# Optimization experiments

Measured on AMD Instinct MI355X. Metric: run time of the kernel, lower is better.

## Reference

```python
import jax, jax.numpy as jnp
import numpy as np

B, S, D, H = 2, 2048, 1024, 16
HD = D // H
NEG_INF = jnp.finfo(jnp.float32).min


def setup_inputs() -> dict:
    key = jax.random.key(0)
    ks = jax.random.split(key, 6)
    s = 1.0 / np.sqrt(D)
    return {
        'x': jax.random.normal(ks[0], (B, S, D), dtype=jnp.float32),
        'Wq': jax.random.normal(ks[1], (D, D), dtype=jnp.float32) * s,
        'Wk': jax.random.normal(ks[2], (D, D), dtype=jnp.float32) * s,
        'Wv': jax.random.normal(ks[3], (D, D), dtype=jnp.float32) * s,
        'Wo': jax.random.normal(ks[4], (D, D), dtype=jnp.float32) * s,
        'bo': jnp.zeros((D,), dtype=jnp.float32),
    }


def reference(x, Wq, Wk, Wv, Wo, bo):
    b, s, _ = x.shape
    scale = HD ** -0.5
    # Q/K/V projections: einsum('bnd,di->bni') == x @ W
    def proj(W):
        return jnp.einsum('bnd,di->bni', x, W).reshape(b, s, H, HD).transpose(0, 2, 1, 3)
    Q, K, V = proj(Wq), proj(Wk), proj(Wv)  # [b,h,s,hd]
    scores = jnp.einsum('bhnd,bhmd->bhnm', Q, K) * scale  # [b,h,s,s]
    causal = jnp.tril(jnp.ones((s, s), dtype=bool))
    scores = jnp.where(causal[None, None], scores, NEG_INF)
    attn = jax.nn.softmax(scores, axis=-1)
    ctx = jnp.einsum('bhnm,bhmd->bhnd', attn, V)
    ctx = ctx.transpose(0, 2, 1, 3).reshape(b, s, D)
    # nn.Linear: ctx @ Wo.T + bo
    return jnp.einsum('bnd,od->bno', ctx, Wo) + bo
```

## Files before the change

kernel.cpp:

```cpp
#include <hip/hip_runtime.h>

#define B_  2
#define S_  2048
#define D_  1024
#define H_  16
#define HD_ 64
#define M_  (B_*S_)

typedef __attribute__((ext_vector_type(8))) short s16x8;
typedef __attribute__((ext_vector_type(4))) float f32x4;
typedef __attribute__((ext_vector_type(16))) float f32x16;

__device__ __forceinline__ unsigned short f2bf(float f) {
  unsigned int u = __builtin_bit_cast(unsigned int, f);
  u += 0x7fffu + ((u >> 16) & 1u);
  return (unsigned short)(u >> 16);
}

__device__ __forceinline__ void gload_lds16(const unsigned short* g, unsigned short* l) {
  __builtin_amdgcn_global_load_lds((const __attribute__((address_space(1))) void*)g,
                                   (__attribute__((address_space(3))) void*)l, 16, 0, 0);
}

__global__ void cvt_kernel(const float* __restrict__ in, unsigned short* __restrict__ out, int n4) {
  int i = blockIdx.x * blockDim.x + threadIdx.x;
  if (i >= n4) return;
  float4 v = reinterpret_cast<const float4*>(in)[i];
  ushort4 o;
  o.x = f2bf(v.x); o.y = f2bf(v.y); o.z = f2bf(v.z); o.w = f2bf(v.w);
  reinterpret_cast<ushort4*>(out)[i] = o;
}

__global__ void transpose_cvt3(const float* __restrict__ W0, const float* __restrict__ W1,
                               const float* __restrict__ W2, unsigned short* __restrict__ dstBase) {
  __shared__ float tile[32][33];
  const float* in = blockIdx.z == 0 ? W0 : (blockIdx.z == 1 ? W1 : W2);
  unsigned short* out = dstBase + (size_t)blockIdx.z * 1024 * 1024;
  const int bx = blockIdx.x, by = blockIdx.y, tx = threadIdx.x;
  const int x = bx * 32 + tx;
  for (int j = threadIdx.y; j < 32; j += 8)
    tile[j][tx] = in[(by * 32 + j) * 1024 + x];
  __syncthreads();
  const int xo = by * 32 + tx;
  for (int j = threadIdx.y; j < 32; j += 8)
    out[(bx * 32 + j) * 1024 + xo] = f2bf(tile[tx][j]);
}

#define BM 128
#define BN 128
#define BK 64

__global__ __launch_bounds__(256, 4) void gemm_bt(
    const unsigned short* __restrict__ A,
    const unsigned short* __restrict__ Bt,
    void* __restrict__ out0, void* __restrict__ out1, void* __restrict__ out2,
    const float* __restrict__ bias,
    const int mode, const float qscale)
{
  __shared__ unsigned short As[BM * BK];
  __shared__ unsigned short Bs[BN * BK];

  const int t    = threadIdx.x;
  const int lane = t & 63;
  const int wid  = t >> 6;
  const int l15  = lane & 15;
  const int g    = lane >> 4;
  const int wm   = wid >> 1;
  const int wn   = wid & 1;

  const int n0 = blockIdx.x * BN;
  const int m0 = blockIdx.y * BM;

  const int lrow = lane >> 3;
  const int lcol = ((lane & 7) ^ lrow) * 8;
  const int rsw  = l15 & 7;

  f32x4 acc[4][4];
#pragma unroll
  for (int i = 0; i < 4; ++i)
#pragma unroll
    for (int j = 0; j < 4; ++j)
      acc[i][j] = (f32x4){0.f, 0.f, 0.f, 0.f};

  for (int kt = 0; kt < 1024 / BK; ++kt) {
    const int k0 = kt * BK;
#pragma unroll
    for (int p = 0; p < 4; ++p) {
      const int c = p * 4 + wid;
      const int row = c * 8 + lrow;
      gload_lds16(&A[(size_t)(m0 + row) * 1024 + k0 + lcol], &As[c * 512]);
      gload_lds16(&Bt[(size_t)(n0 + row) * 1024 + k0 + lcol], &Bs[c * 512]);
    }
    __syncthreads();

#pragma unroll
    for (int kk = 0; kk < 2; ++kk) {
      s16x8 af[4], bf[4];
#pragma unroll
      for (int mi = 0; mi < 4; ++mi)
        af[mi] = *reinterpret_cast<const s16x8*>(
            &As[(wm * 64 + mi * 16 + l15) * BK + (((4 * kk + g) ^ rsw) * 8)]);
#pragma unroll
      for (int ni = 0; ni < 4; ++ni)
        bf[ni] = *reinterpret_cast<const s16x8*>(
            &Bs[(wn * 64 + ni * 16 + l15) * BK + (((4 * kk + g) ^ rsw) * 8)]);
#pragma unroll
      for (int mi = 0; mi < 4; ++mi)
#pragma unroll
        for (int ni = 0; ni < 4; ++ni)
          acc[mi][ni] = __builtin_amdgcn_mfma_f32_16x16x32_bf16(af[mi], bf[ni], acc[mi][ni], 0, 0, 0);
    }
    __syncthreads();
  }

  if (mode == 0) {
    const int sel = n0 >> 10;
    const int nl0 = n0 & 1023;
    if (sel < 2) {
      unsigned short* outb = (unsigned short*)(sel == 0 ? out0 : out1);
      const float sc = (sel == 0) ? qscale : 1.0f;
#pragma unroll
      for (int mi = 0; mi < 4; ++mi) {
#pragma unroll
        for (int ni = 0; ni < 4; ++ni) {
          const int n = nl0 + wn * 64 + ni * 16 + l15;
          const int h = n >> 6, hd = n & 63;
#pragma unroll
          for (int r = 0; r < 4; ++r) {
            const int m = m0 + wm * 64 + mi * 16 + 4 * g + r;
            const int b = m >> 11, s = m & 2047;
            outb[(((b * H_ + h) * S_) + s) * HD_ + hd] = f2bf(acc[mi][ni][r] * sc);
          }
        }
      }
    } else {
      unsigned short* outb = (unsigned short*)out2;
#pragma unroll
      for (int mi = 0; mi < 4; ++mi) {
#pragma unroll
        for (int ni = 0; ni < 4; ++ni) {
          const int n = nl0 + wn * 64 + ni * 16 + l15;
          const int h = n >> 6, hd = n & 63;
          const int m = m0 + wm * 64 + mi * 16 + 4 * g;
          const int b = m >> 11, s = m & 2047;
          ushort4 o;
          o.x = f2bf(acc[mi][ni][0]);
          o.y = f2bf(acc[mi][ni][1]);
          o.z = f2bf(acc[mi][ni][2]);
          o.w = f2bf(acc[mi][ni][3]);
          *reinterpret_cast<ushort4*>(&outb[(((b * H_ + h) * HD_) + hd) * S_ + s]) = o;
        }
      }
    }
  } else {
    float* outf = (float*)out0;
#pragma unroll
    for (int mi = 0; mi < 4; ++mi) {
#pragma unroll
      for (int ni = 0; ni < 4; ++ni) {
        const int n = n0 + wn * 64 + ni * 16 + l15;
        const float bv = bias[n];
#pragma unroll
        for (int r = 0; r < 4; ++r) {
          const int m = m0 + wm * 64 + mi * 16 + 4 * g + r;
          outf[m * 1024 + n] = acc[mi][ni][r] + bv;
        }
      }
    }
  }
}

__global__ __launch_bounds__(256) void attn_kernel(
    const unsigned short* __restrict__ Q,
    const unsigned short* __restrict__ K,
    const unsigned short* __restrict__ VT,
    unsigned short* __restrict__ Ctx)
{
  __shared__ unsigned short Kl[2][64 * 64];
  __shared__ unsigned short Vl[2][64 * 64];
  __shared__ unsigned short Pl[4][2][32][40];

  const int t    = threadIdx.x;
  const int lane = t & 63;
  const int w    = t >> 6;
  const int q    = lane & 31;
  const int hi   = lane >> 5;

  const int bh = blockIdx.x;
  const long base  = (long)bh * S_ * HD_;
  const long vbase = (long)bh * HD_ * S_;

  const int srow = lane >> 3;
  const int scol = ((lane & 7) ^ srow) * 8;
  const int swz  = (q & 7) * 8;

  for (int hp = 0; hp < 2; ++hp) {
    const int qb  = hp == 0 ? 15 - (int)blockIdx.y : (int)blockIdx.y;
    const int q0w = qb * 128 + w * 32;

    s16x8 qf[4];
#pragma unroll
    for (int s = 0; s < 4; ++s)
      qf[s] = *reinterpret_cast<const s16x8*>(&Q[base + (long)(q0w + q) * HD_ + 16 * s + 8 * hi]);

    f32x16 ctx0, ctx1;
#pragma unroll
    for (int r = 0; r < 16; ++r) { ctx0[r] = 0.f; ctx1[r] = 0.f; }
    float m_run = -1e30f, l_run = 0.f;

    const int nt = 2 * qb + 2;

#pragma unroll
    for (int p = 0; p < 2; ++p) {
      const int c = 2 * w + p;
      gload_lds16(&K[base + (long)(c * 8 + srow) * HD_ + scol], &Kl[0][c * 512]);
      gload_lds16(&VT[vbase + (long)(c * 8 + srow) * S_ + scol], &Vl[0][c * 512]);
    }
    __syncthreads();

    for (int kt = 0; kt < nt; ++kt) {
      const int cur  = kt & 1;
      const int kv64 = kt * 64;

      if (kt + 1 < nt) {
        const int nk = kv64 + 64;
#pragma unroll
        for (int p = 0; p < 2; ++p) {
          const int c = 2 * w + p;
          gload_lds16(&K[base + (long)(nk + c * 8 + srow) * HD_ + scol], &Kl[cur ^ 1][c * 512]);
          gload_lds16(&VT[vbase + (long)(c * 8 + srow) * S_ + nk + scol], &Vl[cur ^ 1][c * 512]);
        }
      }

      if (kv64 <= q0w + 31) {
        f32x16 sa0, sa1;
#pragma unroll
        for (int r = 0; r < 16; ++r) { sa0[r] = 0.f; sa1[r] = 0.f; }
        __builtin_amdgcn_s_setprio(1);
#pragma unroll
        for (int s = 0; s < 4; ++s) {
          const s16x8 kb0 = *reinterpret_cast<const s16x8*>(&Kl[cur][(q) * 64 + ((16 * s + 8 * hi) ^ swz)]);
          sa0 = __builtin_amdgcn_mfma_f32_32x32x16_bf16(kb0, qf[s], sa0, 0, 0, 0);
        }
#pragma unroll
        for (int s = 0; s < 4; ++s) {
          const s16x8 kb1 = *reinterpret_cast<const s16x8*>(&Kl[cur][(32 + q) * 64 + ((16 * s + 8 * hi) ^ swz)]);
          sa1 = __builtin_amdgcn_mfma_f32_32x32x16_bf16(kb1, qf[s], sa1, 0, 0, 0);
        }
        __builtin_amdgcn_s_setprio(0);

        if (kv64 + 64 > q0w) {
#pragma unroll
          for (int r = 0; r < 16; ++r) {
            const int kl = (r & 3) + 8 * (r >> 2) + 4 * hi;
            if (kv64 + kl > q0w + q)      sa0[r] = -1e30f;
            if (kv64 + 32 + kl > q0w + q) sa1[r] = -1e30f;
          }
        }

        float mx;
        {
          float a0 = fmaxf(fmaxf(sa0[0], sa0[1]), fmaxf(sa0[2], sa0[3]));
          float a1 = fmaxf(fmaxf(sa0[4], sa0[5]), fmaxf(sa0[6], sa0[7]));
          float a2 = fmaxf(fmaxf(sa0[8], sa0[9]), fmaxf(sa0[10], sa0[11]));
          float a3 = fmaxf(fmaxf(sa0[12], sa0[13]), fmaxf(sa0[14], sa0[15]));
          float b0 = fmaxf(fmaxf(sa1[0], sa1[1]), fmaxf(sa1[2], sa1[3]));
          float b1 = fmaxf(fmaxf(sa1[4], sa1[5]), fmaxf(sa1[6], sa1[7]));
          float b2 = fmaxf(fmaxf(sa1[8], sa1[9]), fmaxf(sa1[10], sa1[11]));
          float b3 = fmaxf(fmaxf(sa1[12], sa1[13]), fmaxf(sa1[14], sa1[15]));
          mx = fmaxf(fmaxf(fmaxf(a0, a1), fmaxf(a2, a3)), fmaxf(fmaxf(b0, b1), fmaxf(b2, b3)));
          mx = fmaxf(mx, __shfl_xor(mx, 32));
        }
        if (mx > m_run + 8.f) {
          const float alpha = __builtin_amdgcn_exp2f(m_run - mx);
          m_run = mx;
          l_run *= alpha;
#pragma unroll
          for (int r = 0; r < 16; ++r) { ctx0[r] *= alpha; ctx1[r] *= alpha; }
        }

        float p0[16], p1[16];
#pragma unroll
        for (int r = 0; r < 16; ++r) {
          p0[r] = __builtin_amdgcn_exp2f(sa0[r] - m_run);
          p1[r] = __builtin_amdgcn_exp2f(sa1[r] - m_run);
        }
        float ps;
        {
          float s0 = ((p0[0] + p0[1]) + (p0[2] + p0[3])) + ((p0[4] + p0[5]) + (p0[6] + p0[7]));
          float s1 = ((p0[8] + p0[9]) + (p0[10] + p0[11])) + ((p0[12] + p0[13]) + (p0[14] + p0[15]));
          float s2 = ((p1[0] + p1[1]) + (p1[2] + p1[3])) + ((p1[4] + p1[5]) + (p1[6] + p1[7]));
          float s3 = ((p1[8] + p1[9]) + (p1[10] + p1[11])) + ((p1[12] + p1[13]) + (p1[14] + p1[15]));
          ps = (s0 + s1) + (s2 + s3);
          ps += __shfl_xor(ps, 32);
        }
        l_run += ps;

#pragma unroll
        for (int c = 0; c < 4; ++c) {
          unsigned int pk01, pk23;
          asm("v_cvt_pk_bf16_f32 %0, %1, %2" : "=v"(pk01) : "v"(p0[4 * c + 0]), "v"(p0[4 * c + 1]));
          asm("v_cvt_pk_bf16_f32 %0, %1, %2" : "=v"(pk23) : "v"(p0[4 * c + 2]), "v"(p0[4 * c + 3]));
          uint2 pr; pr.x = pk01; pr.y = pk23;
          *reinterpret_cast<uint2*>(&Pl[w][0][q][8 * c + 4 * hi]) = pr;
        }
#pragma unroll
        for (int c = 0; c < 4; ++c) {
          unsigned int pk01, pk23;
          asm("v_cvt_pk_bf16_f32 %0, %1, %2" : "=v"(pk01) : "v"(p1[4 * c + 0]), "v"(p1[4 * c + 1]));
          asm("v_cvt_pk_bf16_f32 %0, %1, %2" : "=v"(pk23) : "v"(p1[4 * c + 2]), "v"(p1[4 * c + 3]));
          uint2 pr; pr.x = pk01; pr.y = pk23;
          *reinterpret_cast<uint2*>(&Pl[w][1][q][8 * c + 4 * hi]) = pr;
        }

        __builtin_amdgcn_s_setprio(1);
#pragma unroll
        for (int kc = 0; kc < 4; ++kc) {
          const s16x8 pf = *reinterpret_cast<const s16x8*>(&Pl[w][kc >> 1][q][16 * (kc & 1) + 8 * hi]);
          const s16x8 v0 = *reinterpret_cast<const s16x8*>(&Vl[cur][(q) * 64 + ((16 * kc + 8 * hi) ^ swz)]);
          ctx0 = __builtin_amdgcn_mfma_f32_32x32x16_bf16(v0, pf, ctx0, 0, 0, 0);
          const s16x8 v1 = *reinterpret_cast<const s16x8*>(&Vl[cur][(32 + q) * 64 + ((16 * kc + 8 * hi) ^ swz)]);
          ctx1 = __builtin_amdgcn_mfma_f32_32x32x16_bf16(v1, pf, ctx1, 0, 0, 0);
        }
        __builtin_amdgcn_s_setprio(0);
      }

      __syncthreads();
    }

    const int b = bh >> 4, h = bh & 15;
    const float inv = 1.f / l_run;
    unsigned short* orow = &Ctx[((long)b * S_ + q0w + q) * D_ + h * 64];
#pragma unroll
    for (int c = 0; c < 4; ++c) {
      ushort4 o0, o1;
      o0.x = f2bf(ctx0[4 * c] * inv);     o0.y = f2bf(ctx0[4 * c + 1] * inv);
      o0.z = f2bf(ctx0[4 * c + 2] * inv); o0.w = f2bf(ctx0[4 * c + 3] * inv);
      o1.x = f2bf(ctx1[4 * c] * inv);     o1.y = f2bf(ctx1[4 * c + 1] * inv);
      o1.z = f2bf(ctx1[4 * c + 2] * inv); o1.w = f2bf(ctx1[4 * c + 3] * inv);
      *reinterpret_cast<ushort4*>(&orow[8 * c + 4 * hi])      = o0;
      *reinterpret_cast<ushort4*>(&orow[32 + 8 * c + 4 * hi]) = o1;
    }
  }
}

extern "C" void kernel_launch(void* const* d_in, const int* in_sizes, int n_in,
                              void* d_out, int out_size, void* d_ws, size_t ws_size,
                              hipStream_t stream) {
  const float* x  = (const float*)d_in[0];
  const float* Wq = (const float*)d_in[1];
  const float* Wk = (const float*)d_in[2];
  const float* Wv = (const float*)d_in[3];
  const float* Wo = (const float*)d_in[4];
  const float* bo = (const float*)d_in[5];
  float* out = (float*)d_out;

  char* ws = (char*)d_ws;
  const size_t MB = 1024 * 1024;
  unsigned short* xb  = (unsigned short*)(ws + 0 * MB);
  unsigned short* WT  = (unsigned short*)(ws + 8 * MB);
  unsigned short* Wob = (unsigned short*)(ws + 14 * MB);
  unsigned short* Qb  = (unsigned short*)(ws + 16 * MB);
  unsigned short* Kb  = (unsigned short*)(ws + 24 * MB);
  unsigned short* VTb = (unsigned short*)(ws + 32 * MB);
  unsigned short* Cx  = (unsigned short*)(ws + 40 * MB);

  cvt_kernel<<<(M_ * D_ / 4 + 255) / 256, 256, 0, stream>>>(x, xb, M_ * D_ / 4);
  cvt_kernel<<<(D_ * D_ / 4 + 255) / 256, 256, 0, stream>>>(Wo, Wob, D_ * D_ / 4);
  transpose_cvt3<<<dim3(32, 32, 3), dim3(32, 8), 0, stream>>>(Wq, Wk, Wv, WT);

  gemm_bt<<<dim3(3 * D_ / BN, M_ / BM), 256, 0, stream>>>(
      xb, WT, (void*)Qb, (void*)Kb, (void*)VTb, nullptr, 0, 0.18033688011112042f);

  attn_kernel<<<dim3(B_ * H_, 8), 256, 0, stream>>>(Qb, Kb, VTb, Cx);

  gemm_bt<<<dim3(D_ / BN, M_ / BM), 256, 0, stream>>>(
      Cx, Wob, (void*)out, nullptr, nullptr, bo, 1, 1.0f);
}
```

Measured before the change: 127.9 us.

## Split long causal query blocks across two workgroups with a softmax merge kernel

```diff
diff --git a/kernel.cpp b/kernel.cpp
--- a/kernel.cpp
+++ b/kernel.cpp
@@ -15,6 +15,10 @@
   unsigned int u = __builtin_bit_cast(unsigned int, f);
   u += 0x7fffu + ((u >> 16) & 1u);
   return (unsigned short)(u >> 16);
+}
+__device__ __forceinline__ float bf2f(unsigned short h) {
+  unsigned int u = ((unsigned int)h) << 16;
+  return __builtin_bit_cast(float, u);
 }
 
 __device__ __forceinline__ void gload_lds16(const unsigned short* g, unsigned short* l) {
@@ -174,11 +178,16 @@
     const unsigned short* __restrict__ Q,
     const unsigned short* __restrict__ K,
     const unsigned short* __restrict__ VT,
-    unsigned short* __restrict__ Ctx)
+    unsigned short* __restrict__ Ctx,
+    unsigned short* __restrict__ pctx,
+    float* __restrict__ pml)
 {
   __shared__ unsigned short Kl[2][64 * 64];
   __shared__ unsigned short Vl[2][64 * 64];
   __shared__ unsigned short Pl[4][2][32][40];
+
+  static const unsigned char QBv[24] = {15,15,7,14,14,13,13,6,12,12,11,11,5,10,10,9,9,4,8,8,3,2,1,0};
+  static const signed char   HFv[24] = {0,1,-1,0,1,0,1,-1,0,1,0,1,-1,0,1,0,1,-1,0,1,-1,-1,-1,-1};
 
   const int t    = threadIdx.x;
   const int lane = t & 63;
@@ -187,147 +196,149 @@
   const int hi   = lane >> 5;
 
   const int bh = blockIdx.x;
+  const int qb = QBv[blockIdx.y];
+  const int hf = HFv[blockIdx.y];
   const long base  = (long)bh * S_ * HD_;
   const long vbase = (long)bh * HD_ * S_;
+  const int q0w = qb * 128 + w * 32;
+
+  int ktBeg, ktEnd;
+  if (hf < 0) { ktBeg = 0; ktEnd = 2 * qb + 2; }
+  else        { ktBeg = hf * (qb + 1); ktEnd = ktBeg + qb + 1; }
 
   const int srow = lane >> 3;
   const int scol = ((lane & 7) ^ srow) * 8;
   const int swz  = (q & 7) * 8;
 
-  for (int hp = 0; hp < 2; ++hp) {
-    const int qb  = hp == 0 ? 15 - (int)blockIdx.y : (int)blockIdx.y;
-    const int q0w = qb * 128 + w * 32;
-
-    s16x8 qf[4];
-#pragma unroll
-    for (int s = 0; s < 4; ++s)
-      qf[s] = *reinterpret_cast<const s16x8*>(&Q[base + (long)(q0w + q) * HD_ + 16 * s + 8 * hi]);
-
-    f32x16 ctx0, ctx1;
-#pragma unroll
-    for (int r = 0; r < 16; ++r) { ctx0[r] = 0.f; ctx1[r] = 0.f; }
-    float m_run = -1e30f, l_run = 0.f;
-
-    const int nt = 2 * qb + 2;
-
-#pragma unroll
-    for (int p = 0; p < 2; ++p) {
-      const int c = 2 * w + p;
-      gload_lds16(&K[base + (long)(c * 8 + srow) * HD_ + scol], &Kl[0][c * 512]);
-      gload_lds16(&VT[vbase + (long)(c * 8 + srow) * S_ + scol], &Vl[0][c * 512]);
-    }
+  s16x8 qf[4];
+#pragma unroll
+  for (int s = 0; s < 4; ++s)
+    qf[s] = *reinterpret_cast<const s16x8*>(&Q[base + (long)(q0w + q) * HD_ + 16 * s + 8 * hi]);
+
+  f32x16 ctx0, ctx1;
+#pragma unroll
+  for (int r = 0; r < 16; ++r) { ctx0[r] = 0.f; ctx1[r] = 0.f; }
+  float m_run = -1e30f, l_run = 0.f;
+
+#pragma unroll
+  for (int p = 0; p < 2; ++p) {
+    const int c = 2 * w + p;
+    gload_lds16(&K[base + (long)(ktBeg * 64 + c * 8 + srow) * HD_ + scol], &Kl[0][c * 512]);
+    gload_lds16(&VT[vbase + (long)(c * 8 + srow) * S_ + ktBeg * 64 + scol], &Vl[0][c * 512]);
+  }
+  __syncthreads();
+
+  for (int kt = ktBeg; kt < ktEnd; ++kt) {
+    const int cur  = (kt - ktBeg) & 1;
+    const int kv64 = kt * 64;
+
+    if (kt + 1 < ktEnd) {
+      const int nk = (kt + 1) * 64;
+#pragma unroll
+      for (int p = 0; p < 2; ++p) {
+        const int c = 2 * w + p;
+        gload_lds16(&K[base + (long)(nk + c * 8 + srow) * HD_ + scol], &Kl[cur ^ 1][c * 512]);
+        gload_lds16(&VT[vbase + (long)(c * 8 + srow) * S_ + nk + scol], &Vl[cur ^ 1][c * 512]);
+      }
+    }
+
+    if (kv64 <= q0w + 31) {
+      f32x16 sa0, sa1;
+#pragma unroll
+      for (int r = 0; r < 16; ++r) { sa0[r] = 0.f; sa1[r] = 0.f; }
+      __builtin_amdgcn_s_setprio(1);
+#pragma unroll
+      for (int s = 0; s < 4; ++s) {
+        const s16x8 kb0 = *reinterpret_cast<const s16x8*>(&Kl[cur][(q) * 64 + ((16 * s + 8 * hi) ^ swz)]);
+        sa0 = __builtin_amdgcn_mfma_f32_32x32x16_bf16(kb0, qf[s], sa0, 0, 0, 0);
+      }
+#pragma unroll
+      for (int s = 0; s < 4; ++s) {
+        const s16x8 kb1 = *reinterpret_cast<const s16x8*>(&Kl[cur][(32 + q) * 64 + ((16 * s + 8 * hi) ^ swz)]);
+        sa1 = __builtin_amdgcn_mfma_f32_32x32x16_bf16(kb1, qf[s], sa1, 0, 0, 0);
+      }
+      __builtin_amdgcn_s_setprio(0);
+
+      if (kv64 + 64 > q0w) {
+#pragma unroll
+        for (int r = 0; r < 16; ++r) {
+          const int kl = (r & 3) + 8 * (r >> 2) + 4 * hi;
+          if (kv64 + kl > q0w + q)      sa0[r] = -1e30f;
+          if (kv64 + 32 + kl > q0w + q) sa1[r] = -1e30f;
+        }
+      }
+
+      float mx;
+      {
+        float a0 = fmaxf(fmaxf(sa0[0], sa0[1]), fmaxf(sa0[2], sa0[3]));
+        float a1 = fmaxf(fmaxf(sa0[4], sa0[5]), fmaxf(sa0[6], sa0[7]));
+        float a2 = fmaxf(fmaxf(sa0[8], sa0[9]), fmaxf(sa0[10], sa0[11]));
+        float a3 = fmaxf(fmaxf(sa0[12], sa0[13]), fmaxf(sa0[14], sa0[15]));
+        float b0 = fmaxf(fmaxf(sa1[0], sa1[1]), fmaxf(sa1[2], sa1[3]));
+        float b1 = fmaxf(fmaxf(sa1[4], sa1[5]), fmaxf(sa1[6], sa1[7]));
+        float b2 = fmaxf(fmaxf(sa1[8], sa1[9]), fmaxf(sa1[10], sa1[11]));
+        float b3 = fmaxf(fmaxf(sa1[12], sa1[13]), fmaxf(sa1[14], sa1[15]));
+        mx = fmaxf(fmaxf(fmaxf(a0, a1), fmaxf(a2, a3)), fmaxf(fmaxf(b0, b1), fmaxf(b2, b3)));
+        mx = fmaxf(mx, __shfl_xor(mx, 32));
+      }
+      if (mx > m_run + 8.f) {
+        const float alpha = __builtin_amdgcn_exp2f(m_run - mx);
+        m_run = mx;
+        l_run *= alpha;
+#pragma unroll
+        for (int r = 0; r < 16; ++r) { ctx0[r] *= alpha; ctx1[r] *= alpha; }
+      }
+
+      float p0[16], p1[16];
+#pragma unroll
+      for (int r = 0; r < 16; ++r) {
+        p0[r] = __builtin_amdgcn_exp2f(sa0[r] - m_run);
+        p1[r] = __builtin_amdgcn_exp2f(sa1[r] - m_run);
+      }
+      float ps;
+      {
+        float s0 = ((p0[0] + p0[1]) + (p0[2] + p0[3])) + ((p0[4] + p0[5]) + (p0[6] + p0[7]));
+        float s1 = ((p0[8] + p0[9]) + (p0[10] + p0[11])) + ((p0[12] + p0[13]) + (p0[14] + p0[15]));
+        float s2 = ((p1[0] + p1[1]) + (p1[2] + p1[3])) + ((p1[4] + p1[5]) + (p1[6] + p1[7]));
+        float s3 = ((p1[8] + p1[9]) + (p1[10] + p1[11])) + ((p1[12] + p1[13]) + (p1[14] + p1[15]));
+        ps = (s0 + s1) + (s2 + s3);
+        ps += __shfl_xor(ps, 32);
+      }
+      l_run += ps;
+
+#pragma unroll
+      for (int c = 0; c < 4; ++c) {
+        unsigned int pk01, pk23;
+        asm("v_cvt_pk_bf16_f32 %0, %1, %2" : "=v"(pk01) : "v"(p0[4 * c + 0]), "v"(p0[4 * c + 1]));
+        asm("v_cvt_pk_bf16_f32 %0, %1, %2" : "=v"(pk23) : "v"(p0[4 * c + 2]), "v"(p0[4 * c + 3]));
+        uint2 pr; pr.x = pk01; pr.y = pk23;
+        *reinterpret_cast<uint2*>(&Pl[w][0][q][8 * c + 4 * hi]) = pr;
+      }
+#pragma unroll
+      for (int c = 0; c < 4; ++c) {
+        unsigned int pk01, pk23;
+        asm("v_cvt_pk_bf16_f32 %0, %1, %2" : "=v"(pk01) : "v"(p1[4 * c + 0]), "v"(p1[4 * c + 1]));
+        asm("v_cvt_pk_bf16_f32 %0, %1, %2" : "=v"(pk23) : "v"(p1[4 * c + 2]), "v"(p1[4 * c + 3]));
+        uint2 pr; pr.x = pk01; pr.y = pk23;
+        *reinterpret_cast<uint2*>(&Pl[w][1][q][8 * c + 4 * hi]) = pr;
+      }
+
+      __builtin_amdgcn_s_setprio(1);
+#pragma unroll
+      for (int kc = 0; kc < 4; ++kc) {
+        const s16x8 pf = *reinterpret_cast<const s16x8*>(&Pl[w][kc >> 1][q][16 * (kc & 1) + 8 * hi]);
+        const s16x8 v0 = *reinterpret_cast<const s16x8*>(&Vl[cur][(q) * 64 + ((16 * kc + 8 * hi) ^ swz)]);
+        ctx0 = __builtin_amdgcn_mfma_f32_32x32x16_bf16(v0, pf, ctx0, 0, 0, 0);
+        const s16x8 v1 = *reinterpret_cast<const s16x8*>(&Vl[cur][(32 + q) * 64 + ((16 * kc + 8 * hi) ^ swz)]);
+        ctx1 = __builtin_amdgcn_mfma_f32_32x32x16_bf16(v1, pf, ctx1, 0, 0, 0);
+      }
+      __builtin_amdgcn_s_setprio(0);
+    }
+
     __syncthreads();
-
-    for (int kt = 0; kt < nt; ++kt) {
-      const int cur  = kt & 1;
-      const int kv64 = kt * 64;
-
-      if (kt + 1 < nt) {
-        const int nk = kv64 + 64;
-#pragma unroll
-        for (int p = 0; p < 2; ++p) {
-          const int c = 2 * w + p;
-          gload_lds16(&K[base + (long)(nk + c * 8 + srow) * HD_ + scol], &Kl[cur ^ 1][c * 512]);
-          gload_lds16(&VT[vbase + (long)(c * 8 + srow) * S_ + nk + scol], &Vl[cur ^ 1][c * 512]);
-        }
-      }
-
-      if (kv64 <= q0w + 31) {
-        f32x16 sa0, sa1;
-#pragma unroll
-        for (int r = 0; r < 16; ++r) { sa0[r] = 0.f; sa1[r] = 0.f; }
-        __builtin_amdgcn_s_setprio(1);
-#pragma unroll
-        for (int s = 0; s < 4; ++s) {
-          const s16x8 kb0 = *reinterpret_cast<const s16x8*>(&Kl[cur][(q) * 64 + ((16 * s + 8 * hi) ^ swz)]);
-          sa0 = __builtin_amdgcn_mfma_f32_32x32x16_bf16(kb0, qf[s], sa0, 0, 0, 0);
-        }
-#pragma unroll
-        for (int s = 0; s < 4; ++s) {
-          const s16x8 kb1 = *reinterpret_cast<const s16x8*>(&Kl[cur][(32 + q) * 64 + ((16 * s + 8 * hi) ^ swz)]);
-          sa1 = __builtin_amdgcn_mfma_f32_32x32x16_bf16(kb1, qf[s], sa1, 0, 0, 0);
-        }
-        __builtin_amdgcn_s_setprio(0);
-
-        if (kv64 + 64 > q0w) {
-#pragma unroll
-          for (int r = 0; r < 16; ++r) {
-            const int kl = (r & 3) + 8 * (r >> 2) + 4 * hi;
-            if (kv64 + kl > q0w + q)      sa0[r] = -1e30f;
-            if (kv64 + 32 + kl > q0w + q) sa1[r] = -1e30f;
-          }
-        }
-
-        float mx;
-        {
-          float a0 = fmaxf(fmaxf(sa0[0], sa0[1]), fmaxf(sa0[2], sa0[3]));
-          float a1 = fmaxf(fmaxf(sa0[4], sa0[5]), fmaxf(sa0[6], sa0[7]));
-          float a2 = fmaxf(fmaxf(sa0[8], sa0[9]), fmaxf(sa0[10], sa0[11]));
-          float a3 = fmaxf(fmaxf(sa0[12], sa0[13]), fmaxf(sa0[14], sa0[15]));
-          float b0 = fmaxf(fmaxf(sa1[0], sa1[1]), fmaxf(sa1[2], sa1[3]));
-          float b1 = fmaxf(fmaxf(sa1[4], sa1[5]), fmaxf(sa1[6], sa1[7]));
-          float b2 = fmaxf(fmaxf(sa1[8], sa1[9]), fmaxf(sa1[10], sa1[11]));
-          float b3 = fmaxf(fmaxf(sa1[12], sa1[13]), fmaxf(sa1[14], sa1[15]));
-          mx = fmaxf(fmaxf(fmaxf(a0, a1), fmaxf(a2, a3)), fmaxf(fmaxf(b0, b1), fmaxf(b2, b3)));
-          mx = fmaxf(mx, __shfl_xor(mx, 32));
-        }
-        if (mx > m_run + 8.f) {
-          const float alpha = __builtin_amdgcn_exp2f(m_run - mx);
-          m_run = mx;
-          l_run *= alpha;
-#pragma unroll
-          for (int r = 0; r < 16; ++r) { ctx0[r] *= alpha; ctx1[r] *= alpha; }
-        }
-
-        float p0[16], p1[16];
-#pragma unroll
-        for (int r = 0; r < 16; ++r) {
-          p0[r] = __builtin_amdgcn_exp2f(sa0[r] - m_run);
-          p1[r] = __builtin_amdgcn_exp2f(sa1[r] - m_run);
-        }
-        float ps;
-        {
-          float s0 = ((p0[0] + p0[1]) + (p0[2] + p0[3])) + ((p0[4] + p0[5]) + (p0[6] + p0[7]));
-          float s1 = ((p0[8] + p0[9]) + (p0[10] + p0[11])) + ((p0[12] + p0[13]) + (p0[14] + p0[15]));
-          float s2 = ((p1[0] + p1[1]) + (p1[2] + p1[3])) + ((p1[4] + p1[5]) + (p1[6] + p1[7]));
-          float s3 = ((p1[8] + p1[9]) + (p1[10] + p1[11])) + ((p1[12] + p1[13]) + (p1[14] + p1[15]));
-          ps = (s0 + s1) + (s2 + s3);
-          ps += __shfl_xor(ps, 32);
-        }
-        l_run += ps;
-
-#pragma unroll
-        for (int c = 0; c < 4; ++c) {
-          unsigned int pk01, pk23;
-          asm("v_cvt_pk_bf16_f32 %0, %1, %2" : "=v"(pk01) : "v"(p0[4 * c + 0]), "v"(p0[4 * c + 1]));
-          asm("v_cvt_pk_bf16_f32 %0, %1, %2" : "=v"(pk23) : "v"(p0[4 * c + 2]), "v"(p0[4 * c + 3]));
-          uint2 pr; pr.x = pk01; pr.y = pk23;
-          *reinterpret_cast<uint2*>(&Pl[w][0][q][8 * c + 4 * hi]) = pr;
-        }
-#pragma unroll
-        for (int c = 0; c < 4; ++c) {
-          unsigned int pk01, pk23;
-          asm("v_cvt_pk_bf16_f32 %0, %1, %2" : "=v"(pk01) : "v"(p1[4 * c + 0]), "v"(p1[4 * c + 1]));
-          asm("v_cvt_pk_bf16_f32 %0, %1, %2" : "=v"(pk23) : "v"(p1[4 * c + 2]), "v"(p1[4 * c + 3]));
-          uint2 pr; pr.x = pk01; pr.y = pk23;
-          *reinterpret_cast<uint2*>(&Pl[w][1][q][8 * c + 4 * hi]) = pr;
-        }
-
-        __builtin_amdgcn_s_setprio(1);
-#pragma unroll
-        for (int kc = 0; kc < 4; ++kc) {
-          const s16x8 pf = *reinterpret_cast<const s16x8*>(&Pl[w][kc >> 1][q][16 * (kc & 1) + 8 * hi]);
-          const s16x8 v0 = *reinterpret_cast<const s16x8*>(&Vl[cur][(q) * 64 + ((16 * kc + 8 * hi) ^ swz)]);
-          ctx0 = __builtin_amdgcn_mfma_f32_32x32x16_bf16(v0, pf, ctx0, 0, 0, 0);
-          const s16x8 v1 = *reinterpret_cast<const s16x8*>(&Vl[cur][(32 + q) * 64 + ((16 * kc + 8 * hi) ^ swz)]);
-          ctx1 = __builtin_amdgcn_mfma_f32_32x32x16_bf16(v1, pf, ctx1, 0, 0, 0);
-        }
-        __builtin_amdgcn_s_setprio(0);
-      }
-
-      __syncthreads();
-    }
-
+  }
+
+  if (hf < 0) {
     const int b = bh >> 4, h = bh & 15;
     const float inv = 1.f / l_run;
     unsigned short* orow = &Ctx[((long)b * S_ + q0w + q) * D_ + h * 64];
@@ -341,6 +352,66 @@
       *reinterpret_cast<ushort4*>(&orow[8 * c + 4 * hi])      = o0;
       *reinterpret_cast<ushort4*>(&orow[32 + 8 * c + 4 * hi]) = o1;
     }
+  } else {
+    const int sidx = ((bh << 3) + (qb - 8)) * 2 + hf;
+    const int rloc = w * 32 + q;
+    unsigned short* prow = &pctx[((long)sidx * 128 + rloc) * 64];
+#pragma unroll
+    for (int c = 0; c < 4; ++c) {
+      ushort4 o0, o1;
+      o0.x = f2bf(ctx0[4 * c]);     o0.y = f2bf(ctx0[4 * c + 1]);
+      o0.z = f2bf(ctx0[4 * c + 2]); o0.w = f2bf(ctx0[4 * c + 3]);
+      o1.x = f2bf(ctx1[4 * c]);     o1.y = f2bf(ctx1[4 * c + 1]);
+      o1.z = f2bf(ctx1[4 * c + 2]); o1.w = f2bf(ctx1[4 * c + 3]);
+      *reinterpret_cast<ushort4*>(&prow[8 * c + 4 * hi])      = o0;
+      *reinterpret_cast<ushort4*>(&prow[32 + 8 * c + 4 * hi]) = o1;
+    }
+    if (hi == 0) {
+      pml[((long)sidx * 128 + rloc) * 2]     = m_run;
+      pml[((long)sidx * 128 + rloc) * 2 + 1] = l_run;
+    }
+  }
+}
+
+__global__ __launch_bounds__(256) void merge_kernel(
+    const unsigned short* __restrict__ pctx,
+    const float* __restrict__ pml,
+    unsigned short* __restrict__ Ctx)
+{
+  const int unit = blockIdx.x;
+  const int bh = unit >> 3;
+  const int qb = (unit & 7) + 8;
+  const long s0 = (long)unit * 2, s1 = s0 + 1;
+
+  const int t   = threadIdx.x;
+  const int row = t >> 1;
+  const int hh  = t & 1;
+
+  const long r0 = s0 * 128 + row;
+  const long r1 = s1 * 128 + row;
+  const float m0 = pml[r0 * 2], l0 = pml[r0 * 2 + 1];
+  const float m1 = pml[r1 * 2], l1 = pml[r1 * 2 + 1];
+  const float M  = fmaxf(m0, m1);
+  const float a0 = __builtin_amdgcn_exp2f(m0 - M);
+  const float a1 = __builtin_amdgcn_exp2f(m1 - M);
+  const float inv = 1.f / (l0 * a0 + l1 * a1);
+
+  const unsigned short* c0p = &pctx[r0 * 64 + hh * 32];
+  const unsigned short* c1p = &pctx[r1 * 64 + hh * 32];
+  const int b = bh >> 4, h = bh & 15;
+  unsigned short* op = &Ctx[((long)b * S_ + qb * 128 + row) * D_ + h * 64 + hh * 32];
+
+#pragma unroll
+  for (int j = 0; j < 32; j += 8) {
+    const s16x8 v0 = *reinterpret_cast<const s16x8*>(&c0p[j]);
+    const s16x8 v1 = *reinterpret_cast<const s16x8*>(&c1p[j]);
+    s16x8 o;
+#pragma unroll
+    for (int e = 0; e < 8; ++e) {
+      const float f = (bf2f((unsigned short)v0[e]) * a0 + bf2f((unsigned short)v1[e]) * a1) * inv;
+      o[e] = (short)f2bf(f);
+    }
+    *reinterpret_cast<s16x8*>(&op[j]) = o;
   }
 }
 
@@ -364,6 +435,8 @@
   unsigned short* Kb  = (unsigned short*)(ws + 24 * MB);
   unsigned short* VTb = (unsigned short*)(ws + 32 * MB);
   unsigned short* Cx  = (unsigned short*)(ws + 40 * MB);
+  unsigned short* pctx = (unsigned short*)(ws + 0 * MB);
+  float*          pml  = (float*)(ws + 8 * MB);
 
   cvt_kernel<<<(M_ * D_ / 4 + 255) / 256, 256, 0, stream>>>(x, xb, M_ * D_ / 4);
   cvt_kernel<<<(D_ * D_ / 4 + 255) / 256, 256, 0, stream>>>(Wo, Wob, D_ * D_ / 4);
@@ -372,7 +445,8 @@
   gemm_bt<<<dim3(3 * D_ / BN, M_ / BM), 256, 0, stream>>>(
       xb, WT, (void*)Qb, (void*)Kb, (void*)VTb, nullptr, 0, 0.18033688011112042f);
 
-  attn_kernel<<<dim3(B_ * H_, 8), 256, 0, stream>>>(Qb, Kb, VTb, Cx);
+  attn_kernel<<<dim3(B_ * H_, 24), 256, 0, stream>>>(Qb, Kb, VTb, Cx, pctx, pml);
+  merge_kernel<<<256, 256, 0, stream>>>(pctx, pml, Cx);
 
   gemm_bt<<<dim3(D_ / BN, M_ / BM), 256, 0, stream>>>(
       Cx, Wob, (void*)out, nullptr, nullptr, bo, 1, 1.0f);
```

Result: faster. 116.4 us (median of 4 runs) (-9.0%).
